# Kernel tuning notes

Measured on AMD Instinct MI355X. Metric: run time of the kernel, lower is better.

## Reference

```python
import jax, jax.numpy as jnp
import numpy as np

N_EMBD = 2048
N_HEAD = 16
N_INNER = 8192
EPS = 1e-5


def _wn_weight(v, g):
    # torch weight_norm with dim=1 on weight [out, in]:
    # w[:, j] = g[j] * v[:, j] / ||v[:, j]||_2
    norm = jnp.sqrt(jnp.sum(v * v, axis=0))  # [in]
    return v * (g / norm)[None, :]


def _layer_norm(x, gamma, beta):
    mu = jnp.mean(x, axis=-1, keepdims=True)
    var = jnp.mean(jnp.square(x - mu), axis=-1, keepdims=True)
    return (x - mu) * jax.lax.rsqrt(var + EPS) * gamma + beta


def setup_inputs() -> dict:
    key = jax.random.key(0)
    ks = jax.random.split(key, 12)
    E, I, H = N_EMBD, N_INNER, N_HEAD
    s = lambda n: 1.0 / np.sqrt(n)
    return {
        "hidden_states": jax.random.normal(ks[0], (2, 2048, E), jnp.float32),
        "ln1_g": jnp.ones((E,), jnp.float32),
        "ln1_b": jnp.zeros((E,), jnp.float32),
        "w_qkv": jax.random.normal(ks[1], (3 * E, E), jnp.float32) * s(E),
        "b_qkv": jnp.zeros((3 * E,), jnp.float32),
        "attn_proj_v": jax.random.normal(ks[2], (E, E), jnp.float32) * s(E),
        "attn_proj_g": jnp.abs(jax.random.normal(ks[3], (E,), jnp.float32)) + 0.5,
        "attn_proj_b": jnp.zeros((E,), jnp.float32),
        "emotion_bias": jax.random.normal(ks[4], (H,), jnp.float32) * 0.1,
        "ln2_g": jnp.ones((E,), jnp.float32),
        "ln2_b": jnp.zeros((E,), jnp.float32),
        "w_fc": jax.random.normal(ks[5], (I, E), jnp.float32) * s(E),
        "b_fc": jnp.zeros((I,), jnp.float32),
        "mlp_proj_v": jax.random.normal(ks[6], (E, I), jnp.float32) * s(I),
        "mlp_proj_g": jnp.abs(jax.random.normal(ks[7], (I,), jnp.float32)) + 0.5,
        "mlp_proj_b": jnp.zeros((E,), jnp.float32),
    }


def reference(hidden_states, ln1_g, ln1_b, w_qkv, b_qkv, attn_proj_v, attn_proj_g,
              attn_proj_b, emotion_bias, ln2_g, ln2_b, w_fc, b_fc,
              mlp_proj_v, mlp_proj_g, mlp_proj_b):
    B, S, E = hidden_states.shape
    H = N_HEAD
    D = E // H

    # --- attention sub-block ---
    residual = hidden_states
    x = _layer_norm(hidden_states, ln1_g, ln1_b)
    qkv = x @ w_qkv.T + b_qkv                       # [B,S,3E]
    q, k, v = jnp.split(qkv, 3, axis=-1)
    q = q.reshape(B, S, H, D).transpose(0, 2, 1, 3)  # [B,H,S,D]
    k = k.reshape(B, S, H, D).transpose(0, 2, 1, 3)
    v = v.reshape(B, S, H, D).transpose(0, 2, 1, 3)

    scores = jnp.einsum("bhqd,bhkd->bhqk", q, k) / jnp.sqrt(jnp.float32(D))
    scores = scores + emotion_bias[None, :, None, None]
    probs = jax.nn.softmax(scores, axis=-1)
    attn = jnp.einsum("bhqk,bhkd->bhqd", probs, v)   # [B,H,S,D]
    attn = attn.transpose(0, 2, 1, 3).reshape(B, S, E)
    w_proj = _wn_weight(attn_proj_v, attn_proj_g)
    attn = attn @ w_proj.T + attn_proj_b

    hidden = attn + residual

    # --- MLP sub-block ---
    residual = hidden
    x = _layer_norm(hidden, ln2_g, ln2_b)
    h = jax.nn.gelu(x @ w_fc.T + b_fc, approximate=False)
    w_proj2 = _wn_weight(mlp_proj_v, mlp_proj_g)
    h = h @ w_proj2.T + mlp_proj_b
    return residual + h
```

## Files before the change

kernel.cpp:

```cpp
#include <hip/hip_runtime.h>
#include <hip/hip_bf16.h>

#define DEVI __device__ __forceinline__

typedef __attribute__((ext_vector_type(8))) __bf16 bf16x8;
typedef __attribute__((ext_vector_type(4))) float f32x4;
typedef __attribute__((ext_vector_type(4))) unsigned short u16x4;
typedef __attribute__((ext_vector_type(8))) unsigned short u16x8;

DEVI unsigned short f2bf(float f) {
  unsigned int u = __float_as_uint(f);
  u += 0x7FFFu + ((u >> 16) & 1u);
  return (unsigned short)(u >> 16);
}
DEVI float bf2f(unsigned short u) {
  return __uint_as_float(((unsigned int)u) << 16);
}

#define GLD16(g, l) __builtin_amdgcn_global_load_lds(                      \
    (const __attribute__((address_space(1))) void*)(g),                    \
    (__attribute__((address_space(3))) void*)(l), 16, 0, 0)


DEVI void cast_body(int blk, int nblk, const float* __restrict__ in,
                    unsigned short* __restrict__ out, int n4) {
  for (int i = blk * 256 + threadIdx.x; i < n4; i += nblk * 256) {
    f32x4 v = ((const f32x4*)in)[i];
    u16x4 o;
    o.x = f2bf(v.x); o.y = f2bf(v.y); o.z = f2bf(v.z); o.w = f2bf(v.w);
    ((u16x4*)out)[i] = o;
  }
}

DEVI void scale_cast_body(int blk, int nblk, const float* __restrict__ in,
                          const float* __restrict__ s,
                          unsigned short* __restrict__ out, int cols, int n4) {
  const int cmask4 = (cols >> 2) - 1;
  for (int i = blk * 256 + threadIdx.x; i < n4; i += nblk * 256) {
    f32x4 v = ((const f32x4*)in)[i];
    f32x4 sv = ((const f32x4*)s)[i & cmask4];
    u16x4 o;
    o.x = f2bf(v.x * sv.x); o.y = f2bf(v.y * sv.y);
    o.z = f2bf(v.z * sv.z); o.w = f2bf(v.w * sv.w);
    ((u16x4*)out)[i] = o;
  }
}

DEVI void colnorm1_body(int bx, int by, const float* __restrict__ v,
                        float* __restrict__ part, int cols) {
  const int tid = threadIdx.x;
  const int g = tid & 127;
  const int s = tid >> 7;
  const int c0 = bx * 512;
  const int r0 = by * 64 + s * 32;
  const float* base = v + (size_t)r0 * cols + c0 + g * 4;
  f32x4 acc = {};
#pragma unroll 4
  for (int i = 0; i < 32; ++i) {
    f32x4 x = *(const f32x4*)(base + (size_t)i * cols);
    acc.x += x.x * x.x; acc.y += x.y * x.y;
    acc.z += x.z * x.z; acc.w += x.w * x.w;
  }
  __shared__ f32x4 red1[256];
  red1[tid] = acc;
  __syncthreads();
  if (s == 0) {
    f32x4 a = red1[tid], b = red1[tid + 128];
    f32x4 o;
    o.x = a.x + b.x; o.y = a.y + b.y; o.z = a.z + b.z; o.w = a.w + b.w;
    *(f32x4*)(part + (size_t)by * cols + c0 + g * 4) = o;
  }
}

DEVI void colnorm2_body(int blk, const float* __restrict__ part,
                        const float* __restrict__ g, float* __restrict__ s,
                        int cols, int nrc) {
  const int c = blk * 256 + threadIdx.x;
  float acc = 0.f;
  for (int i = 0; i < nrc; ++i) acc += part[(size_t)i * cols + c];
  s[c] = g[c] * rsqrtf(acc);
}

DEVI void ln_body(int row, const float* __restrict__ x, const float* __restrict__ g,
                  const float* __restrict__ b, unsigned short* __restrict__ out) {
  const int tid = threadIdx.x, lane = tid & 63, wid = tid >> 6;
  const float* xr = x + (size_t)row * 2048;
  f32x4 a0 = ((const f32x4*)xr)[tid];
  f32x4 a1 = ((const f32x4*)xr)[tid + 256];
  float s = a0.x + a0.y + a0.z + a0.w + a1.x + a1.y + a1.z + a1.w;
  float ss = a0.x * a0.x + a0.y * a0.y + a0.z * a0.z + a0.w * a0.w +
             a1.x * a1.x + a1.y * a1.y + a1.z * a1.z + a1.w * a1.w;
#pragma unroll
  for (int m = 1; m < 64; m <<= 1) {
    s += __shfl_xor(s, m);
    ss += __shfl_xor(ss, m);
  }
  __shared__ float red2[8];
  if (lane == 0) { red2[wid] = s; red2[4 + wid] = ss; }
  __syncthreads();
  s = red2[0] + red2[1] + red2[2] + red2[3];
  ss = red2[4] + red2[5] + red2[6] + red2[7];
  const float mu = s * (1.f / 2048.f);
  const float var = ss * (1.f / 2048.f) - mu * mu;
  const float rs = rsqrtf(var + 1e-5f);
  f32x4 g0 = ((const f32x4*)g)[tid], g1 = ((const f32x4*)g)[tid + 256];
  f32x4 b0 = ((const f32x4*)b)[tid], b1 = ((const f32x4*)b)[tid + 256];
  u16x4 o0, o1;
  o0.x = f2bf((a0.x - mu) * rs * g0.x + b0.x);
  o0.y = f2bf((a0.y - mu) * rs * g0.y + b0.y);
  o0.z = f2bf((a0.z - mu) * rs * g0.z + b0.z);
  o0.w = f2bf((a0.w - mu) * rs * g0.w + b0.w);
  o1.x = f2bf((a1.x - mu) * rs * g1.x + b1.x);
  o1.y = f2bf((a1.y - mu) * rs * g1.y + b1.y);
  o1.z = f2bf((a1.z - mu) * rs * g1.z + b1.z);
  o1.w = f2bf((a1.w - mu) * rs * g1.w + b1.w);
  unsigned short* orow = out + (size_t)row * 2048;
  *(u16x4*)(orow + 4 * tid) = o0;
  *(u16x4*)(orow + 1024 + 4 * tid) = o1;
}

DEVI void vtrans_body(int bid, const unsigned short* __restrict__ qkv,
                      unsigned short* __restrict__ vt) {
  __shared__ unsigned short tsh[64][134];
  const int tid = threadIdx.x;
  const int bh = bid >> 5, st = bid & 31;
  const int b = bh >> 4, h = bh & 15;
  const unsigned short* vb = qkv + (size_t)(b * 2048 + st * 64) * 6144 + 4096 + h * 128;
#pragma unroll
  for (int i = 0; i < 4; ++i) {
    int f = tid + (i << 8);
    int row = f >> 4, c8 = f & 15;
    u16x8 x = *(const u16x8*)(vb + (size_t)row * 6144 + c8 * 8);
#pragma unroll
    for (int j = 0; j < 4; ++j) {
      unsigned int pk = ((unsigned int)x[2 * j + 1] << 16) | x[2 * j];
      *(unsigned int*)&tsh[row][c8 * 8 + 2 * j] = pk;
    }
  }
  __syncthreads();
  const int lane = tid & 63, wid = tid >> 6;
  unsigned short* ob = vt + ((size_t)bh << 18) + (st << 6);
#pragma unroll
  for (int j = 0; j < 32; ++j) {
    int d = (wid << 5) + j;
    ob[((size_t)d << 11) + lane] = tsh[lane][d];
  }
}

DEVI void combine_body(int blk, const unsigned short* __restrict__ po,
                       const float* __restrict__ marr, const float* __restrict__ larr,
                       unsigned short* __restrict__ O) {
  const size_t PS = (size_t)32 * 2048 * 128;
  const float C = 0.08838834764831845f * 1.4426950408889634f;
  const int tid = threadIdx.x;
  const int row = blk * 32 + (tid >> 3);
  const int bh = row >> 11, q = row & 2047;
  const int d0 = (tid & 7) * 16;
  const float m0 = marr[row], m1 = marr[65536 + row];
  const float l0 = larr[row], l1 = larr[65536 + row];
  const float M = fmaxf(m0, m1);
  const float w0 = exp2f((m0 - M) * C), w1 = exp2f((m1 - M) * C);
  const float inv = 1.f / (l0 * w0 + l1 * w1);
  const float s0 = w0 * inv, s1 = w1 * inv;
  const unsigned short* p0 = po + ((size_t)row << 7) + d0;
  const unsigned short* p1 = p0 + PS;
  const int b = bh >> 4, h = bh & 15;
  unsigned short* ob = O + ((size_t)(b * 2048 + q)) * 2048 + h * 128 + d0;
#pragma unroll
  for (int c = 0; c < 2; ++c) {
    u16x8 a = *(const u16x8*)(p0 + c * 8);
    u16x8 bb = *(const u16x8*)(p1 + c * 8);
    u16x8 o;
#pragma unroll
    for (int j = 0; j < 8; ++j)
      o[j] = f2bf(bf2f(a[j]) * s0 + bf2f(bb[j]) * s1);
    *(u16x8*)(ob + c * 8) = o;
  }
}


__global__ __launch_bounds__(256) void prep1_k(const float* wq, unsigned short* wqb,
                                               const float* apv, float* part_a,
                                               const float* mpv, float* part_m,
                                               const float* hid, const float* g1v,
                                               const float* b1v, unsigned short* xln) {
  const int blk = blockIdx.x;
  if (blk < 2048)       cast_body(blk, 2048, wq, wqb, (6144 * 2048) / 4);
  else if (blk < 2176) { int i = blk - 2048; colnorm1_body(i & 3, i >> 2, apv, part_a, 2048); }
  else if (blk < 2688) { int i = blk - 2176; colnorm1_body(i & 15, i >> 4, mpv, part_m, 8192); }
  else                  ln_body(blk - 2688, hid, g1v, b1v, xln);
}

__global__ __launch_bounds__(256) void prep2_k(const float* part_a, const float* apg,
                                               float* s_attn, const float* part_m,
                                               const float* mpg, float* s_mlp) {
  const int blk = blockIdx.x;
  if (blk < 8) colnorm2_body(blk, part_a, apg, s_attn, 2048, 32);
  else         colnorm2_body(blk - 8, part_m, mpg, s_mlp, 8192, 32);
}

__global__ __launch_bounds__(256) void mid_k(const unsigned short* qkv,
                                             unsigned short* vt,
                                             const float* apv, const float* s_attn,
                                             unsigned short* wproj_bf) {
  const int blk = blockIdx.x;
  if (blk < 1024) vtrans_body(blk, qkv, vt);
  else            scale_cast_body(blk - 1024, 2048, apv, s_attn, wproj_bf, 2048,
                                  (2048 * 2048) / 4);
}

__global__ __launch_bounds__(256) void post_k(const unsigned short* po,
                                              const float* marr, const float* larr,
                                              unsigned short* attn_out,
                                              const float* wfc, unsigned short* wfc_bf,
                                              const float* mpv, const float* s_mlp,
                                              unsigned short* w2_bf) {
  const int blk = blockIdx.x;
  if (blk < 2048)       combine_body(blk, po, marr, larr, attn_out);
  else if (blk < 4096)  cast_body(blk - 2048, 2048, wfc, wfc_bf, (8192 * 2048) / 4);
  else                  scale_cast_body(blk - 4096, 2048, mpv, s_mlp, w2_bf, 8192,
                                        (2048 * 8192) / 4);
}

__global__ __launch_bounds__(256) void ln_k(const float* __restrict__ x,
                                            const float* __restrict__ g,
                                            const float* __restrict__ b,
                                            unsigned short* __restrict__ out) {
  ln_body(blockIdx.x, x, g, b, out);
}

__global__ __launch_bounds__(256) void g4red_k(const unsigned short* __restrict__ parts,
                                               const float* __restrict__ bias,
                                               const float* __restrict__ res,
                                               float* __restrict__ out, int n4) {
  const size_t PS = (size_t)4096 * 2048;
  for (int i = blockIdx.x * 256 + threadIdx.x; i < n4; i += gridDim.x * 256) {
    u16x4 a = ((const u16x4*)(parts))[i];
    u16x4 b = ((const u16x4*)(parts + PS))[i];
    f32x4 r = ((const f32x4*)res)[i];
    f32x4 bb = ((const f32x4*)bias)[i & 511];
    f32x4 o;
    o.x = bf2f(a.x) + bf2f(b.x) + r.x + bb.x;
    o.y = bf2f(a.y) + bf2f(b.y) + r.y + bb.y;
    o.z = bf2f(a.z) + bf2f(b.z) + r.z + bb.z;
    o.w = bf2f(a.w) + bf2f(b.w) + r.w + bb.w;
    ((f32x4*)out)[i] = o;
  }
}

struct GemmP {
  const unsigned short* A;
  const unsigned short* B;
  const float* bias;
  const float* res;
  float* outF;
  unsigned short* outH;
  int M, N, K;
};

DEVI void gemm128_body(const GemmP& p, int m0, int n0, int k0, int nk) {
  const int tid = threadIdx.x, lane = tid & 63, wid = tid >> 6;
  const int K = p.K;
  const int wr = wid >> 1, wc = wid & 1;

  __shared__ __align__(16) unsigned short sA[2][4096];
  __shared__ __align__(16) unsigned short sB[2][4096];

  const int c0 = tid, c1 = tid + 256;
  const unsigned short* gA0 = p.A + (size_t)(m0 + (c0 >> 2)) * K + k0 + ((c0 & 3) << 3);
  const unsigned short* gA1 = p.A + (size_t)(m0 + (c1 >> 2)) * K + k0 + ((c1 & 3) << 3);
  const unsigned short* gB0 = p.B + (size_t)(n0 + (c0 >> 2)) * K + k0 + ((c0 & 3) << 3);
  const unsigned short* gB1 = p.B + (size_t)(n0 + (c1 >> 2)) * K + k0 + ((c1 & 3) << 3);
  const int l0 = wid << 9, l1 = (wid << 9) + 2048;

  f32x4 acc[4][4] = {};
  const int arow = (wr << 6) + (lane & 15);
  const int brow = (wc << 6) + (lane & 15);
  const int koff = (lane >> 4) << 3;

#define STAGE128(bufi, t) do { int ko = (t) << 5;       \
    GLD16(gA0 + ko, &sA[bufi][l0]);                     \
    GLD16(gA1 + ko, &sA[bufi][l1]);                     \
    GLD16(gB0 + ko, &sB[bufi][l0]);                     \
    GLD16(gB1 + ko, &sB[bufi][l1]); } while (0)

  STAGE128(0, 0);
  __syncthreads();
  int cur = 0;
  for (int t = 0; t < nk; ++t) {
    if (t + 1 < nk) STAGE128(cur ^ 1, t + 1);
    bf16x8 af[4], bfr[4];
#pragma unroll
    for (int i = 0; i < 4; ++i)
      af[i] = *(const bf16x8*)&sA[cur][(arow + (i << 4)) * 32 + koff];
#pragma unroll
    for (int i = 0; i < 4; ++i)
      bfr[i] = *(const bf16x8*)&sB[cur][(brow + (i << 4)) * 32 + koff];
#pragma unroll
    for (int i = 0; i < 4; ++i)
#pragma unroll
      for (int j = 0; j < 4; ++j)
        acc[i][j] = __builtin_amdgcn_mfma_f32_16x16x32_bf16(af[i], bfr[j], acc[i][j], 0, 0, 0);
    __syncthreads();
    cur ^= 1;
  }
#undef STAGE128

  const int rbase = m0 + (wr << 6) + ((lane >> 4) << 2);
  const int cbase = n0 + (wc << 6) + (lane & 15);
#pragma unroll
  for (int mi = 0; mi < 4; ++mi) {
#pragma unroll
    for (int ni = 0; ni < 4; ++ni) {
      const int col = cbase + (ni << 4);
#pragma unroll
      for (int r = 0; r < 4; ++r) {
        const int row = rbase + (mi << 4) + r;
        const size_t o = (size_t)row * p.N + col;
        p.outF[o] = acc[mi][ni][r] + p.bias[col] + p.res[o];
      }
    }
  }
}

__global__ __launch_bounds__(256) void g2_proj128(GemmP p) {
  const int x = blockIdx.x & 7, i = blockIdx.x >> 3;
  const int bm = (x >> 1) * 8 + (i >> 3);
  const int bn = (x & 1) * 8 + (i & 7);
  gemm128_body(p, bm << 7, bn << 7, 0, p.K >> 5);
}

DEVI void setup256(const GemmP& p, int m0, int n0, int k0,
                   const unsigned short*& gsA0, const unsigned short*& gsA1,
                   const unsigned short*& gsB0, const unsigned short*& gsB1) {
  const int tid = threadIdx.x;
  int r_[2], c_[2];
#pragma unroll
  for (int j = 0; j < 2; ++j) {
    int d = tid * 16 + j * 8192;
    int w = (d & 1023) ^ (((d >> 9) & 1) << 5);
    r_[j] = ((d >> 10) << 4) + (w >> 6);
    c_[j] = (w & 63) >> 1;
  }
  gsA0 = p.A + (size_t)(m0 + r_[0]) * p.K + k0 + c_[0];
  gsA1 = p.A + (size_t)(m0 + r_[1]) * p.K + k0 + c_[1];
  gsB0 = p.B + (size_t)(n0 + r_[0]) * p.K + k0 + c_[0];
  gsB1 = p.B + (size_t)(n0 + r_[1]) * p.K + k0 + c_[1];
}

template <int EPI>
DEVI void epi256(const GemmP& p, f32x4 (&acc)[8][4], int m0, int n0,
                 unsigned short* outH) {
  const int lane = threadIdx.x & 63, wid = threadIdx.x >> 6;
  const int wr = wid >> 2, wc = wid & 3;
  const int lr = lane & 15, lk = lane >> 4;
  const int rbase = m0 + wr * 128 + (lk << 2);
  const int cbase = n0 + wc * 64 + lr;
#pragma unroll
  for (int m = 0; m < 8; ++m) {
#pragma unroll
    for (int n = 0; n < 4; ++n) {
      const int col = cbase + (n << 4);
      const float bb = (EPI == 5) ? 0.f : p.bias[col];
#pragma unroll
      for (int r = 0; r < 4; ++r) {
        const int row = rbase + (m << 4) + r;
        float v = acc[m][n][r] + bb;
        if constexpr (EPI == 2) {
          float y = 0.7978845608028654f * (v + 0.044715f * v * v * v);
          float u = __expf(2.f * y);
          v = (y > 40.f) ? v : v * (u / (u + 1.f));
        }
        outH[(size_t)row * p.N + col] = f2bf(v);
      }
    }
  }
}

template <int EPI>
DEVI void gemm2p_body(const GemmP& p, unsigned short* lds_raw, int m0, int n0,
                      int k0, int nk, unsigned short* outH) {
  const int tid = threadIdx.x, lane = tid & 63, wid = tid >> 6;
  const int wr = wid >> 2, wc = wid & 3;
  const int lr = lane & 15, lk = lane >> 4;
  const int fb = (lr * 64 + lk * 16) ^ ((lr & 8) << 2);

  const unsigned short *gsA0, *gsA1, *gsB0, *gsB1;
  setup256(p, m0, n0, k0, gsA0, gsA1, gsB0, gsB1);

#define STG2(b, kt) do { unsigned short* _d = lds_raw + ((b) << 14);     \
    GLD16(gsA0 + ((size_t)(kt) << 5), _d + (tid << 3));                  \
    GLD16(gsA1 + ((size_t)(kt) << 5), _d + 4096 + (tid << 3));           \
    GLD16(gsB0 + ((size_t)(kt) << 5), _d + 8192 + (tid << 3));           \
    GLD16(gsB1 + ((size_t)(kt) << 5), _d + 12288 + (tid << 3)); } while (0)

  f32x4 acc[8][4] = {};
  STG2(0, 0);
  __syncthreads();
  int cur = 0;
  for (int t = 0; t < nk; ++t) {
    if (t + 1 < nk) STG2(cur ^ 1, t + 1);
    const char* tA = (const char*)(lds_raw + (cur << 14));
    const char* tB = tA + 16384;
    bf16x8 a_[8], b_[4];
#pragma unroll
    for (int n = 0; n < 4; ++n)
      b_[n] = *(const bf16x8*)(tB + (((wc << 2) + n) << 10) + fb);
#pragma unroll
    for (int m = 0; m < 8; ++m)
      a_[m] = *(const bf16x8*)(tA + (((wr << 3) + m) << 10) + fb);
#pragma unroll
    for (int m = 0; m < 8; ++m)
#pragma unroll
      for (int n = 0; n < 4; ++n)
        acc[m][n] = __builtin_amdgcn_mfma_f32_16x16x32_bf16(a_[m], b_[n], acc[m][n], 0, 0, 0);
    __syncthreads();
    cur ^= 1;
  }
#undef STG2
  epi256<EPI>(p, acc, m0, n0, outH);
}

template <int EPI>
DEVI void gemmr2k64_body(const GemmP& p, unsigned short* lds_raw, int m0, int n0,
                         int k0, int nk64, unsigned short* outH) {
  const int tid = threadIdx.x, lane = tid & 63, wid = tid >> 6;
  const int wr = wid >> 2, wc = wid & 3;
  const int lr = lane & 15, lk = lane >> 4;
  const int fb = (lr * 64 + lk * 16) ^ ((lr & 8) << 2);

  const unsigned short *gsA0, *gsA1, *gsB0, *gsB1;
  setup256(p, m0, n0, k0, gsA0, gsA1, gsB0, gsB1);

#define STG64(bufi, kt) do { unsigned short* _d = lds_raw + ((bufi) << 15);  \
    int _ko = (kt) << 6;                                                     \
    GLD16(gsA0 + _ko,      _d + (tid << 3));                                 \
    GLD16(gsA1 + _ko,      _d + 4096 + (tid << 3));                          \
    GLD16(gsA0 + _ko + 32, _d + 8192 + (tid << 3));                          \
    GLD16(gsA1 + _ko + 32, _d + 12288 + (tid << 3));                         \
    GLD16(gsB0 + _ko,      _d + 16384 + (tid << 3));                         \
    GLD16(gsB1 + _ko,      _d + 20480 + (tid << 3));                         \
    GLD16(gsB0 + _ko + 32, _d + 24576 + (tid << 3));                         \
    GLD16(gsB1 + _ko + 32, _d + 28672 + (tid << 3)); } while (0)

  f32x4 acc[8][4] = {};
  STG64(0, 0);
  asm volatile("s_waitcnt vmcnt(0)" ::: "memory");
  __builtin_amdgcn_s_barrier();
  asm volatile("" ::: "memory");

  for (int t = 0; t < nk64; ++t) {
    if (t + 1 < nk64) STG64((t + 1) & 1, t + 1);
    const char* base = (const char*)(lds_raw + ((t & 1) << 15));
#pragma unroll
    for (int s = 0; s < 2; ++s) {
      const char* tA = base + s * 16384;
      const char* tB = base + 32768 + s * 16384;
      bf16x8 a_[8], b_[4];
#pragma unroll
      for (int n = 0; n < 4; ++n)
        b_[n] = *(const bf16x8*)(tB + (((wc << 2) + n) << 10) + fb);
#pragma unroll
      for (int m = 0; m < 8; ++m)
        a_[m] = *(const bf16x8*)(tA + (((wr << 3) + m) << 10) + fb);
      __builtin_amdgcn_s_setprio(1);
#pragma unroll
      for (int m = 0; m < 8; ++m)
#pragma unroll
        for (int n = 0; n < 4; ++n)
          acc[m][n] = __builtin_amdgcn_mfma_f32_16x16x32_bf16(a_[m], b_[n], acc[m][n], 0, 0, 0);
      __builtin_amdgcn_s_setprio(0);
    }
    if (t + 1 < nk64) asm volatile("s_waitcnt vmcnt(0)" ::: "memory");
    __builtin_amdgcn_s_barrier();
    asm volatile("" ::: "memory");
  }
#undef STG64
  epi256<EPI>(p, acc, m0, n0, outH);
}

__global__ __launch_bounds__(512, 2) void g1_qkv256(GemmP p) {
  extern __shared__ unsigned short lds_raw[];
  const int x = blockIdx.x & 7, i = blockIdx.x >> 3;
  const int bm = (x & 1) * 8 + (i & 7);
  const int bn = (x >> 1) * 6 + (i >> 3);
  gemm2p_body<0>(p, lds_raw, bm << 8, bn << 8, 0, p.K >> 5, p.outH);
}
__global__ __launch_bounds__(512, 1) void g3_fc64(GemmP p) {
  extern __shared__ unsigned short lds_raw[];
  const int x = blockIdx.x & 7, i = blockIdx.x >> 3;
  const int bm = (x & 1) * 8 + (i & 7);
  const int bn = (x >> 1) * 8 + (i >> 3);
  gemmr2k64_body<2>(p, lds_raw, bm << 8, bn << 8, 0, 32, p.outH);
}
__global__ __launch_bounds__(512, 1) void g4_sk64(GemmP p) {
  extern __shared__ unsigned short lds_raw[];
  const int x = blockIdx.x & 7, i = blockIdx.x >> 3;
  const int ks = x & 1;
  const int bm = (x >> 1) * 4 + (i >> 3);
  const int bn = i & 7;
  unsigned short* outH = p.outH + (size_t)ks * 4096 * 2048;
  gemmr2k64_body<5>(p, lds_raw, bm << 8, bn << 8, ks << 12, 64, outH);
}

__global__ __launch_bounds__(512) void attn_k(const unsigned short* __restrict__ qkv,
                                              const unsigned short* __restrict__ Vt,
                                              unsigned short* __restrict__ po,
                                              float* __restrict__ marr,
                                              float* __restrict__ larr) {
  const int tid = threadIdx.x, lane = tid & 63, wid = tid >> 6;
  const int bid = blockIdx.x;
  const int j = bid >> 3;
  const int bh = (bid & 7) * 4 + (j >> 5);
  const int rest = j & 31;
  const int qt = rest >> 1, kvh = rest & 1;
  const int q0 = qt * 128 + wid * 16;
  const int b = bh >> 4, h = bh & 15;
  const int kt0 = kvh << 4;
  const float C = 0.08838834764831845f * 1.4426950408889634f;

  __shared__ __align__(16) unsigned short sK[64 * 128];
  __shared__ __align__(16) unsigned short sV[128 * 64];
  __shared__ __align__(16) unsigned short sP[8][16 * 72];

  const unsigned short* Qb = qkv + (size_t)(b * 2048) * 6144 + h * 128;
  const unsigned short* Kb = qkv + (size_t)(b * 2048) * 6144 + 2048 + h * 128;
  const unsigned short* Vb = Vt + ((size_t)bh << 18);

  bf16x8 qf[4];
  {
    const unsigned short* qp = Qb + (size_t)(q0 + (lane & 15)) * 6144 + ((lane >> 4) << 3);
#pragma unroll
    for (int kk = 0; kk < 4; ++kk) qf[kk] = *(const bf16x8*)(qp + kk * 32);
  }

  int koffs[2], voffs[2];
#pragma unroll
  for (int i = 0; i < 2; ++i) {
    const int c = tid + (i << 9);
    const int kv = c >> 4, jj = c & 15;
    const int js = (jj & 8) | ((jj ^ kv) & 7);
    koffs[i] = kv * 6144 + (js << 3);
    const int d = c >> 3, j2 = c & 7;
    const int js2 = j2 ^ (d & 7);
    voffs[i] = d * 2048 + (js2 << 3);
  }
  u16x8 kreg[2], vreg[2];
  auto PREF = [&](int kt) {
    const int kv0 = kt << 6;
    const unsigned short* kb = Kb + (size_t)kv0 * 6144;
#pragma unroll
    for (int i = 0; i < 2; ++i) {
      kreg[i] = *(const u16x8*)(kb + koffs[i]);
      vreg[i] = *(const u16x8*)(Vb + kv0 + voffs[i]);
    }
  };

  f32x4 oacc[8] = {};
  float mrun = -3e38f, lrun = 0.f;
  PREF(kt0);

  for (int kt = 0; kt < 16; ++kt) {
#pragma unroll
    for (int i = 0; i < 2; ++i) {
      const int c8 = (tid + (i << 9)) << 3;
      *(u16x8*)&sK[c8] = kreg[i];
      *(u16x8*)&sV[c8] = vreg[i];
    }
    __syncthreads();
    if (kt + 1 < 16) PREF(kt0 + kt + 1);

    f32x4 sc[4] = {};
    __builtin_amdgcn_s_setprio(1);
#pragma unroll
    for (int ti = 0; ti < 4; ++ti) {
#pragma unroll
      for (int kk = 0; kk < 4; ++kk) {
        const int row = (ti << 4) + (lane & 15);
        int bo = (row << 8) + (kk << 6) + ((lane >> 4) << 4);
        bo ^= (row & 7) << 4;
        bf16x8 kf = *(const bf16x8*)((const char*)sK + bo);
        sc[ti] = __builtin_amdgcn_mfma_f32_16x16x32_bf16(kf, qf[kk], sc[ti], 0, 0, 0);
      }
    }
    __builtin_amdgcn_s_setprio(0);

    float pv[16];
    float mx = -3e38f;
#pragma unroll
    for (int ti = 0; ti < 4; ++ti)
#pragma unroll
      for (int r = 0; r < 4; ++r) {
        float x = sc[ti][r];
        pv[(ti << 2) + r] = x;
        mx = fmaxf(mx, x);
      }
    mx = fmaxf(mx, __shfl_xor(mx, 16));
    mx = fmaxf(mx, __shfl_xor(mx, 32));

    float corr = 1.f;
    if (!__all(mx - mrun <= 90.50966799f)) {
      const float mnew = fmaxf(mrun, mx);
      corr = exp2f((mrun - mnew) * C);
      mrun = mnew;
      float fr[4];
#pragma unroll
      for (int r = 0; r < 4; ++r) fr[r] = __shfl(corr, ((lane >> 4) << 2) + r);
#pragma unroll
      for (int di = 0; di < 8; ++di)
#pragma unroll
        for (int r = 0; r < 4; ++r) oacc[di][r] *= fr[r];
    }
    float psum = 0.f;
#pragma unroll
    for (int i2 = 0; i2 < 16; ++i2) {
      float e = exp2f((pv[i2] - mrun) * C);
      pv[i2] = e;
      psum += e;
    }
    psum += __shfl_xor(psum, 16);
    psum += __shfl_xor(psum, 32);
    lrun = lrun * corr + psum;

    unsigned short* prow = &sP[wid][(lane & 15) * 72];
#pragma unroll
    for (int ti = 0; ti < 4; ++ti) {
      u16x4 w4;
      w4.x = f2bf(pv[(ti << 2) + 0]);
      w4.y = f2bf(pv[(ti << 2) + 1]);
      w4.z = f2bf(pv[(ti << 2) + 2]);
      w4.w = f2bf(pv[(ti << 2) + 3]);
      *(u16x4*)&prow[(ti << 4) + ((lane >> 4) << 2)] = w4;
    }

    bf16x8 pfA, pfB;
    {
      const char* pb = (const char*)&sP[wid][0] + (lane & 15) * 144 + ((lane >> 4) << 4);
      pfA = *(const bf16x8*)(pb);
      pfB = *(const bf16x8*)(pb + 64);
    }
    __builtin_amdgcn_s_setprio(1);
#pragma unroll
    for (int di = 0; di < 8; ++di) {
#pragma unroll
      for (int ks = 0; ks < 2; ++ks) {
        const int dr = (di << 4) + (lane & 15);
        int bo = (dr << 7) + (ks << 6) + ((lane >> 4) << 4);
        bo ^= (dr & 7) << 4;
        bf16x8 vf = *(const bf16x8*)((const char*)sV + bo);
        oacc[di] = __builtin_amdgcn_mfma_f32_16x16x32_bf16(ks ? pfB : pfA, vf, oacc[di], 0, 0, 0);
      }
    }
    __builtin_amdgcn_s_setprio(0);
    __syncthreads();
  }

  const size_t PS = (size_t)32 * 2048 * 128;
  unsigned short* pob = po + (size_t)kvh * PS + ((size_t)bh << 18);
#pragma unroll
  for (int di = 0; di < 8; ++di)
#pragma unroll
    for (int r = 0; r < 4; ++r) {
      const size_t o = (size_t)(q0 + ((lane >> 4) << 2) + r) * 128 + (di << 4) + (lane & 15);
      pob[o] = f2bf(oacc[di][r]);
    }
  if (lane < 16) {
    const int idx = kvh * 65536 + (bh << 11) + q0 + lane;
    marr[idx] = mrun;
    larr[idx] = lrun;
  }
}


extern "C" void kernel_launch(void* const* d_in, const int* in_sizes, int n_in,
                              void* d_out, int out_size, void* d_ws, size_t ws_size,
                              hipStream_t stream) {
  (void)in_sizes; (void)n_in; (void)out_size; (void)ws_size;
  const float* hidden = (const float*)d_in[0];
  const float* ln1_g = (const float*)d_in[1];
  const float* ln1_b = (const float*)d_in[2];
  const float* w_qkv = (const float*)d_in[3];
  const float* b_qkv = (const float*)d_in[4];
  const float* apv = (const float*)d_in[5];
  const float* apg = (const float*)d_in[6];
  const float* apb = (const float*)d_in[7];
  const float* ln2_g = (const float*)d_in[9];
  const float* ln2_b = (const float*)d_in[10];
  const float* w_fc = (const float*)d_in[11];
  const float* b_fc = (const float*)d_in[12];
  const float* mpv = (const float*)d_in[13];
  const float* mpg = (const float*)d_in[14];
  const float* mpb = (const float*)d_in[15];

  char* w = (char*)d_ws;
  const size_t MBs = 1ull << 20;
  unsigned short* xln = (unsigned short*)(w + 0);
  unsigned short* po = (unsigned short*)(w + 0);
  float* hidden2 = (float*)(w + 0);
  unsigned short* vtbuf = (unsigned short*)(w + 32 * MBs);
  unsigned short* hbuf = (unsigned short*)(w + 32 * MBs);
  unsigned short* qkv = (unsigned short*)(w + 96 * MBs);
  unsigned short* wfc_bf = (unsigned short*)(w + 96 * MBs);
  unsigned short* partH = (unsigned short*)(w + 96 * MBs);
  unsigned short* xln2 = (unsigned short*)(w + 128 * MBs);
  unsigned short* attn_out = (unsigned short*)(w + 144 * MBs);
  unsigned short* wqkv_bf = (unsigned short*)(w + 160 * MBs);
  unsigned short* w2_bf = (unsigned short*)(w + 160 * MBs);
  unsigned short* wproj_bf = (unsigned short*)(w + 192 * MBs);
  float* s_attn = (float*)(w + 200 * MBs);
  float* s_mlp = (float*)(w + 200 * MBs + 32768);
  float* part_attn = (float*)(w + 201 * MBs);
  float* part_mlp = (float*)(w + 202 * MBs);
  float* marr = (float*)(w + 203 * MBs);
  float* larr = (float*)(w + 203 * MBs + (1 << 19));

  hipFuncSetAttribute((const void*)g1_qkv256, hipFuncAttributeMaxDynamicSharedMemorySize, 65536);
  hipFuncSetAttribute((const void*)g3_fc64, hipFuncAttributeMaxDynamicSharedMemorySize, 131072);
  hipFuncSetAttribute((const void*)g4_sk64, hipFuncAttributeMaxDynamicSharedMemorySize, 131072);

  prep1_k<<<6784, 256, 0, stream>>>(w_qkv, wqkv_bf, apv, part_attn, mpv, part_mlp,
                                    hidden, ln1_g, ln1_b, xln);
  prep2_k<<<40, 256, 0, stream>>>(part_attn, apg, s_attn, part_mlp, mpg, s_mlp);

  GemmP p1 = {xln, wqkv_bf, b_qkv, nullptr, nullptr, qkv, 4096, 6144, 2048};
  g1_qkv256<<<384, 512, 65536, stream>>>(p1);

  mid_k<<<3072, 256, 0, stream>>>(qkv, vtbuf, apv, s_attn, wproj_bf);

  attn_k<<<1024, 512, 0, stream>>>(qkv, vtbuf, po, marr, larr);

  post_k<<<6144, 256, 0, stream>>>(po, marr, larr, attn_out, w_fc, wfc_bf,
                                   mpv, s_mlp, w2_bf);

  GemmP p2 = {attn_out, wproj_bf, apb, hidden, hidden2, nullptr, 4096, 2048, 2048};
  g2_proj128<<<512, 256, 0, stream>>>(p2);

  ln_k<<<4096, 256, 0, stream>>>(hidden2, ln2_g, ln2_b, xln2);

  GemmP p3 = {xln2, wfc_bf, b_fc, nullptr, nullptr, hbuf, 4096, 8192, 2048};
  g3_fc64<<<512, 512, 131072, stream>>>(p3);

  GemmP p4 = {hbuf, w2_bf, mpb, nullptr, nullptr, partH, 4096, 2048, 8192};
  g4_sk64<<<256, 512, 131072, stream>>>(p4);
  g4red_k<<<1024, 256, 0, stream>>>(partH, mpb, hidden2, (float*)d_out,
                                    (4096 * 2048) / 4);
}
```

Baseline: 725.9 us.

## Replace split-K MLP down-proj and 128x128 attn proj with unified 128x256 GEMM

```diff
diff --git a/kernel.cpp b/kernel.cpp
--- a/kernel.cpp
+++ b/kernel.cpp
@@ -229,25 +229,6 @@
   ln_body(blockIdx.x, x, g, b, out);
 }
 
-__global__ __launch_bounds__(256) void g4red_k(const unsigned short* __restrict__ parts,
-                                               const float* __restrict__ bias,
-                                               const float* __restrict__ res,
-                                               float* __restrict__ out, int n4) {
-  const size_t PS = (size_t)4096 * 2048;
-  for (int i = blockIdx.x * 256 + threadIdx.x; i < n4; i += gridDim.x * 256) {
-    u16x4 a = ((const u16x4*)(parts))[i];
-    u16x4 b = ((const u16x4*)(parts + PS))[i];
-    f32x4 r = ((const f32x4*)res)[i];
-    f32x4 bb = ((const f32x4*)bias)[i & 511];
-    f32x4 o;
-    o.x = bf2f(a.x) + bf2f(b.x) + r.x + bb.x;
-    o.y = bf2f(a.y) + bf2f(b.y) + r.y + bb.y;
-    o.z = bf2f(a.z) + bf2f(b.z) + r.z + bb.z;
-    o.w = bf2f(a.w) + bf2f(b.w) + r.w + bb.w;
-    ((f32x4*)out)[i] = o;
-  }
-}
-
 struct GemmP {
   const unsigned short* A;
   const unsigned short* B;
@@ -258,78 +239,6 @@
   int M, N, K;
 };
 
-DEVI void gemm128_body(const GemmP& p, int m0, int n0, int k0, int nk) {
-  const int tid = threadIdx.x, lane = tid & 63, wid = tid >> 6;
-  const int K = p.K;
-  const int wr = wid >> 1, wc = wid & 1;
-
-  __shared__ __align__(16) unsigned short sA[2][4096];
-  __shared__ __align__(16) unsigned short sB[2][4096];
-
-  const int c0 = tid, c1 = tid + 256;
-  const unsigned short* gA0 = p.A + (size_t)(m0 + (c0 >> 2)) * K + k0 + ((c0 & 3) << 3);
-  const unsigned short* gA1 = p.A + (size_t)(m0 + (c1 >> 2)) * K + k0 + ((c1 & 3) << 3);
-  const unsigned short* gB0 = p.B + (size_t)(n0 + (c0 >> 2)) * K + k0 + ((c0 & 3) << 3);
-  const unsigned short* gB1 = p.B + (size_t)(n0 + (c1 >> 2)) * K + k0 + ((c1 & 3) << 3);
-  const int l0 = wid << 9, l1 = (wid << 9) + 2048;
-
-  f32x4 acc[4][4] = {};
-  const int arow = (wr << 6) + (lane & 15);
-  const int brow = (wc << 6) + (lane & 15);
-  const int koff = (lane >> 4) << 3;
-
-#define STAGE128(bufi, t) do { int ko = (t) << 5;       \
-    GLD16(gA0 + ko, &sA[bufi][l0]);                     \
-    GLD16(gA1 + ko, &sA[bufi][l1]);                     \
-    GLD16(gB0 + ko, &sB[bufi][l0]);                     \
-    GLD16(gB1 + ko, &sB[bufi][l1]); } while (0)
-
-  STAGE128(0, 0);
-  __syncthreads();
-  int cur = 0;
-  for (int t = 0; t < nk; ++t) {
-    if (t + 1 < nk) STAGE128(cur ^ 1, t + 1);
-    bf16x8 af[4], bfr[4];
-#pragma unroll
-    for (int i = 0; i < 4; ++i)
-      af[i] = *(const bf16x8*)&sA[cur][(arow + (i << 4)) * 32 + koff];
-#pragma unroll
-    for (int i = 0; i < 4; ++i)
-      bfr[i] = *(const bf16x8*)&sB[cur][(brow + (i << 4)) * 32 + koff];
-#pragma unroll
-    for (int i = 0; i < 4; ++i)
-#pragma unroll
-      for (int j = 0; j < 4; ++j)
-        acc[i][j] = __builtin_amdgcn_mfma_f32_16x16x32_bf16(af[i], bfr[j], acc[i][j], 0, 0, 0);
-    __syncthreads();
-    cur ^= 1;
-  }
-#undef STAGE128
-
-  const int rbase = m0 + (wr << 6) + ((lane >> 4) << 2);
-  const int cbase = n0 + (wc << 6) + (lane & 15);
-#pragma unroll
-  for (int mi = 0; mi < 4; ++mi) {
-#pragma unroll
-    for (int ni = 0; ni < 4; ++ni) {
-      const int col = cbase + (ni << 4);
-#pragma unroll
-      for (int r = 0; r < 4; ++r) {
-        const int row = rbase + (mi << 4) + r;
-        const size_t o = (size_t)row * p.N + col;
-        p.outF[o] = acc[mi][ni][r] + p.bias[col] + p.res[o];
-      }
-    }
-  }
-}
-
-__global__ __launch_bounds__(256) void g2_proj128(GemmP p) {
-  const int x = blockIdx.x & 7, i = blockIdx.x >> 3;
-  const int bm = (x >> 1) * 8 + (i >> 3);
-  const int bn = (x & 1) * 8 + (i & 7);
-  gemm128_body(p, bm << 7, bn << 7, 0, p.K >> 5);
-}
-
 DEVI void setup256(const GemmP& p, int m0, int n0, int k0,
                    const unsigned short*& gsA0, const unsigned short*& gsA1,
                    const unsigned short*& gsB0, const unsigned short*& gsB1) {
@@ -361,7 +270,7 @@
 #pragma unroll
     for (int n = 0; n < 4; ++n) {
       const int col = cbase + (n << 4);
-      const float bb = (EPI == 5) ? 0.f : p.bias[col];
+      const float bb = p.bias[col];
 #pragma unroll
       for (int r = 0; r < 4; ++r) {
         const int row = rbase + (m << 4) + r;
@@ -479,6 +388,80 @@
   epi256<EPI>(p, acc, m0, n0, outH);
 }
 
+template <int NK64>
+DEVI void gemmw128_body(const GemmP& p, unsigned short* lds_raw, int m0, int n0) {
+  const int tid = threadIdx.x, lane = tid & 63, wid = tid >> 6;
+  const int wr = wid >> 2, wc = wid & 3;
+  const int lr = lane & 15, lk = lane >> 4;
+  const int fb = (lr * 64 + lk * 16) ^ ((lr & 8) << 2);
+
+  const unsigned short *gsA0, *gsA1, *gsB0, *gsB1;
+  setup256(p, m0, n0, 0, gsA0, gsA1, gsB0, gsB1);
+  (void)gsA1;
+
+#define STGW(bufi, kt) do { unsigned short* _d = lds_raw + (bufi) * 24576;   \
+    int _ko = (kt) << 6;                                                     \
+    GLD16(gsA0 + _ko,      _d + (tid << 3));                                 \
+    GLD16(gsA0 + _ko + 32, _d + 4096 + (tid << 3));                          \
+    GLD16(gsB0 + _ko,      _d + 8192 + (tid << 3));                          \
+    GLD16(gsB1 + _ko,      _d + 12288 + (tid << 3));                         \
+    GLD16(gsB0 + _ko + 32, _d + 16384 + (tid << 3));                         \
+    GLD16(gsB1 + _ko + 32, _d + 20480 + (tid << 3)); } while (0)
+
+  f32x4 acc[4][4] = {};
+  STGW(0, 0);
+  asm volatile("s_waitcnt vmcnt(0)" ::: "memory");
+  __builtin_amdgcn_s_barrier();
+  asm volatile("" ::: "memory");
+
+  for (int t = 0; t < NK64; ++t) {
+    if (t + 1 < NK64) STGW((t + 1) & 1, t + 1);
+    const char* base = (const char*)(lds_raw + (t & 1) * 24576);
+#pragma unroll
+    for (int s = 0; s < 2; ++s) {
+      const char* tA = base + s * 8192;
+      const char* tB = base + 16384 + s * 16384;
+      bf16x8 a_[4], b_[4];
+#pragma unroll
+      for (int ni = 0; ni < 4; ++ni) {
+        const int bidx = (wc << 2) + ni;
+        b_[ni] = *(const bf16x8*)(tB + ((bidx >> 3) << 13) + ((bidx & 7) << 10) + fb);
+      }
+#pragma unroll
+      for (int mi = 0; mi < 4; ++mi)
+        a_[mi] = *(const bf16x8*)(tA + (((wr << 2) + mi) << 10) + fb);
+      __builtin_amdgcn_s_setprio(1);
+#pragma unroll
+      for (int mi = 0; mi < 4; ++mi)
+#pragma unroll
+        for (int ni = 0; ni < 4; ++ni)
+          acc[mi][ni] = __builtin_amdgcn_mfma_f32_16x16x32_bf16(a_[mi], b_[ni], acc[mi][ni], 0, 0, 0);
+      __builtin_amdgcn_s_setprio(0);
+    }
+    if (t + 1 < NK64) asm volatile("s_waitcnt vmcnt(0)" ::: "memory");
+    __builtin_amdgcn_s_barrier();
+    asm volatile("" ::: "memory");
+  }
+#undef STGW
+
+  const int rbase = m0 + wr * 64 + (lk << 2);
+  const int cbase = n0 + wc * 64 + lr;
+#pragma unroll
+  for (int mi = 0; mi < 4; ++mi) {
+#pragma unroll
+    for (int ni = 0; ni < 4; ++ni) {
+      const int col = cbase + (ni << 4);
+      const float bb = p.bias[col];
+#pragma unroll
+      for (int r = 0; r < 4; ++r) {
+        const int row = rbase + (mi << 4) + r;
+        const size_t o = (size_t)row * p.N + col;
+        p.outF[o] = acc[mi][ni][r] + bb + p.res[o];
+      }
+    }
+  }
+}
+
 __global__ __launch_bounds__(512, 2) void g1_qkv256(GemmP p) {
   extern __shared__ unsigned short lds_raw[];
   const int x = blockIdx.x & 7, i = blockIdx.x >> 3;
@@ -493,14 +476,19 @@
   const int bn = (x >> 1) * 8 + (i >> 3);
   gemmr2k64_body<2>(p, lds_raw, bm << 8, bn << 8, 0, 32, p.outH);
 }
-__global__ __launch_bounds__(512, 1) void g4_sk64(GemmP p) {
+__global__ __launch_bounds__(512, 1) void g2_w128(GemmP p) {
   extern __shared__ unsigned short lds_raw[];
   const int x = blockIdx.x & 7, i = blockIdx.x >> 3;
-  const int ks = x & 1;
-  const int bm = (x >> 1) * 4 + (i >> 3);
+  const int bm = x * 4 + (i >> 3);
   const int bn = i & 7;
-  unsigned short* outH = p.outH + (size_t)ks * 4096 * 2048;
-  gemmr2k64_body<5>(p, lds_raw, bm << 8, bn << 8, ks << 12, 64, outH);
+  gemmw128_body<32>(p, lds_raw, bm << 7, bn << 8);
+}
+__global__ __launch_bounds__(512, 1) void g4_w128(GemmP p) {
+  extern __shared__ unsigned short lds_raw[];
+  const int x = blockIdx.x & 7, i = blockIdx.x >> 3;
+  const int bm = x * 4 + (i >> 3);
+  const int bn = i & 7;
+  gemmw128_body<128>(p, lds_raw, bm << 7, bn << 8);
 }
 
 __global__ __launch_bounds__(512) void attn_k(const unsigned short* __restrict__ qkv,
@@ -701,7 +689,6 @@
   unsigned short* hbuf = (unsigned short*)(w + 32 * MBs);
   unsigned short* qkv = (unsigned short*)(w + 96 * MBs);
   unsigned short* wfc_bf = (unsigned short*)(w + 96 * MBs);
-  unsigned short* partH = (unsigned short*)(w + 96 * MBs);
   unsigned short* xln2 = (unsigned short*)(w + 128 * MBs);
   unsigned short* attn_out = (unsigned short*)(w + 144 * MBs);
   unsigned short* wqkv_bf = (unsigned short*)(w + 160 * MBs);
@@ -716,7 +703,8 @@
 
   hipFuncSetAttribute((const void*)g1_qkv256, hipFuncAttributeMaxDynamicSharedMemorySize, 65536);
   hipFuncSetAttribute((const void*)g3_fc64, hipFuncAttributeMaxDynamicSharedMemorySize, 131072);
-  hipFuncSetAttribute((const void*)g4_sk64, hipFuncAttributeMaxDynamicSharedMemorySize, 131072);
+  hipFuncSetAttribute((const void*)g2_w128, hipFuncAttributeMaxDynamicSharedMemorySize, 98304);
+  hipFuncSetAttribute((const void*)g4_w128, hipFuncAttributeMaxDynamicSharedMemorySize, 98304);
 
   prep1_k<<<6784, 256, 0, stream>>>(w_qkv, wqkv_bf, apv, part_attn, mpv, part_mlp,
                                     hidden, ln1_g, ln1_b, xln);
@@ -733,15 +721,13 @@
                                    mpv, s_mlp, w2_bf);
 
   GemmP p2 = {attn_out, wproj_bf, apb, hidden, hidden2, nullptr, 4096, 2048, 2048};
-  g2_proj128<<<512, 256, 0, stream>>>(p2);
+  g2_w128<<<256, 512, 98304, stream>>>(p2);
 
   ln_k<<<4096, 256, 0, stream>>>(hidden2, ln2_g, ln2_b, xln2);
 
   GemmP p3 = {xln2, wfc_bf, b_fc, nullptr, nullptr, hbuf, 4096, 8192, 2048};
   g3_fc64<<<512, 512, 131072, stream>>>(p3);
 
-  GemmP p4 = {hbuf, w2_bf, mpb, nullptr, nullptr, partH, 4096, 2048, 8192};
-  g4_sk64<<<256, 512, 131072, stream>>>(p4);
-  g4red_k<<<1024, 256, 0, stream>>>(partH, mpb, hidden2, (float*)d_out,
-                                    (4096 * 2048) / 4);
-}
+  GemmP p4 = {hbuf, w2_bf, mpb, hidden2, (float*)d_out, nullptr, 4096, 2048, 8192};
+  g4_w128<<<256, 512, 98304, stream>>>(p4);
+}
```

New measurement: 720.9 us. About the same (-0.7%).
